# Performance work log

Hardware: AMD Instinct MI355X
Metric: run time of the kernel (lower is better)

The kernel has to match this reference:

```python
import jax, jax.numpy as jnp
import numpy as np

# Hypernetwork config (matches init_kwargs)
INP = 4096      # inp_size
MSK = 64        # mask_size
HID = 64        # node_hidden_size (target-net hidden)
OUT = 10        # out_size (target outputs)
L1, L2, L3 = 64, 256, 128  # hypernet trunk layers
B = 16384       # batch
WVEC = MSK * HID + HID + HID * OUT + OUT  # 4810 generated weights per sample


def _linear_params(key, fan_in, fan_out):
    # torch.nn.Linear default init: U(-1/sqrt(fan_in), 1/sqrt(fan_in))
    lim = 1.0 / np.sqrt(fan_in)
    kw, kb = jax.random.split(key)
    W = jax.random.uniform(kw, (fan_out, fan_in), minval=-lim, maxval=lim, dtype=jnp.float32)
    b = jax.random.uniform(kb, (fan_out,), minval=-lim, maxval=lim, dtype=jnp.float32)
    return W, b


def setup_inputs() -> dict:
    key = jax.random.key(0)
    ks = jax.random.split(key, 6)
    W1, b1 = _linear_params(ks[0], INP, L1)
    W2, b2 = _linear_params(ks[1], L1, L2)
    W3, b3 = _linear_params(ks[2], L2, L3)
    W4, b4 = _linear_params(ks[3], L3, WVEC)
    data = jax.random.normal(ks[4], (B, INP), dtype=jnp.float32)
    mask_idx = jnp.sort(jax.random.randint(ks[5], (B, MSK), 0, INP), axis=1)  # int indices of active features
    return dict(data=data, mask_idx=mask_idx,
                W1=W1, b1=b1, W2=W2, b2=b2, W3=W3, b3=b3, W4=W4, b4=b4)


def reference(data, mask_idx, W1, b1, W2, b2, W3, b3, W4, b4):
    b = data.shape[0]
    # Rebuild the float binary mask [B, INP] from indices (scatter ones)
    rows = jnp.arange(b)[:, None]
    mask = jnp.zeros((b, INP), dtype=data.dtype).at[rows, mask_idx].set(1.0)

    # craft_network: 4-layer MLP on the mask (dropout is identity in eval / for reference)
    h = jax.nn.relu(mask @ W1.T + b1)
    h = jax.nn.relu(h @ W2.T + b2)
    h = jax.nn.relu(h @ W3.T + b3)
    w = h @ W4.T + b4  # [B, WVEC] generated weights per sample

    # Split per-sample generated weights (same layout as InsertableNet)
    iw_end = MSK * HID
    ib_end = iw_end + HID
    ow_end = ib_end + HID * OUT
    inp_w = w[:, :iw_end].reshape(b, HID, MSK)       # [B, H, M]
    inp_b = w[:, iw_end:ib_end]                      # [B, H]
    out_w = w[:, ib_end:ow_end].reshape(b, OUT, HID) # [B, O, H]
    out_b = w[:, ow_end:]                            # [B, O]

    # Per-sample gather of masked features: data[i, mask[i]] -> [B, M]
    xm = jnp.take_along_axis(data, mask_idx, axis=1)

    # Batched tiny 2-layer MLP (replaces the per-sample Python loop)
    hid = jax.nn.relu(jnp.einsum('bhm,bm->bh', inp_w, xm) + inp_b)
    res = jnp.einsum('boh,bh->bo', out_w, hid) + out_b  # [B, OUT]
    return res
```

## Files before the change

### kernel.cpp

```cpp
#include <hip/hip_runtime.h>


typedef _Float16 f16;
typedef _Float16 f16x8 __attribute__((ext_vector_type(8)));
typedef _Float16 f16x4 __attribute__((ext_vector_type(4)));
typedef float    f32x4 __attribute__((ext_vector_type(4)));

#define NPAD 4864

__global__ __launch_bounds__(256) void k_prep(
    const float* __restrict__ W1, const float* __restrict__ W2,
    const float* __restrict__ W3, const float* __restrict__ W4,
    f16* __restrict__ W1Th, f16* __restrict__ W2h,
    f16* __restrict__ W3h, f16* __restrict__ W4s)
{
    const int tid = blockIdx.x * 256 + threadIdx.x;
    const int stride = gridDim.x * 256;
    for (int e = tid; e < 4096 * 64; e += stride) {
        int j = e >> 6, i = e & 63;
        W1Th[e] = (f16)W1[(size_t)i * 4096 + j];
    }
    for (int e = tid; e < NPAD * 128; e += stride) {
        const int j    = e & 7;
        const int lane = (e >> 3) & 63;
        const int mt   = (e >> 9) & 3;
        const int kk   = (e >> 11) & 3;
        const int c    = e >> 13;
        const int lr = lane & 15, g = lane >> 4;
        const int row = 64 * c + 16 * mt + lr;
        const int col = 32 * kk + 8 * g + j;
        W4s[e] = (row < 4810) ? (f16)W4[(size_t)row * 128 + col] : (f16)0.f;
    }
    for (int e = tid; e < 256 * 64; e += stride)  W2h[e] = (f16)W2[e];
    for (int e = tid; e < 128 * 256; e += stride) W3h[e] = (f16)W3[e];
}

__global__ __launch_bounds__(512, 2) void k_main(
    const float* __restrict__ data, const int* __restrict__ midx,
    const f16* __restrict__ W1Th, const float* __restrict__ b1,
    const f16* __restrict__ W2h, const float* __restrict__ b2,
    const f16* __restrict__ W3h, const float* __restrict__ b3,
    const f16* __restrict__ W4s, const float* __restrict__ b4,
    float* __restrict__ out)
{
    __shared__ __align__(16) char uMain[40960];
    __shared__ __align__(16) char uB[17408];
    __shared__ __align__(16) char uC[17408];
    __shared__ __align__(16) float res_s[64 * 12];

    const int t = threadIdx.x, w = t >> 6, lane = t & 63;
    const int lr = lane & 15, g = lane >> 4;
    const int row0 = blockIdx.x * 64;
    const f32x4 zero = {0.f, 0.f, 0.f, 0.f};

    int*   idx_s = (int*)uB;
    char*  h2b   = uMain;
    char*  h1b   = uMain + 32768;
    char*  h3b   = uC;
    float* xm_s  = (float*)uB;
    float* hid_s = (float*)uC;

    for (int e = t; e < 4096; e += 512)
        idx_s[e] = midx[(size_t)row0 * 64 + e];
    __syncthreads();

    float xr[8];
    #pragma unroll
    for (int k = 0; k < 8; ++k) {
        const int e = k * 512 + t;
        xr[k] = data[(size_t)(row0 + (e >> 6)) * 4096 + idx_s[e]];
    }

    {
        const f32x4 b1v = *(const f32x4*)&b1[lr * 4];
        for (int p = 0; p < 4; ++p) {
            const int s0 = 8 * w + 2 * p, s1 = s0 + 1;
            f32x4 a0 = zero, a1 = zero;
            #pragma unroll
            for (int tt = 0; tt < 16; ++tt) {
                const int i = g * 16 + tt;
                const int c0 = idx_s[s0 * 64 + i];
                const int q0 = (i > 0) ? idx_s[s0 * 64 + i - 1] : -1;
                const int c1 = idx_s[s1 * 64 + i];
                const int q1 = (i > 0) ? idx_s[s1 * 64 + i - 1] : -1;
                const f16x4 w0 = *(const f16x4*)&W1Th[c0 * 64 + lr * 4];
                const f16x4 w1 = *(const f16x4*)&W1Th[c1 * 64 + lr * 4];
                #pragma unroll
                for (int q = 0; q < 4; ++q) {
                    a0[q] += (c0 != q0) ? (float)w0[q] : 0.f;
                    a1[q] += (c1 != q1) ? (float)w1[q] : 0.f;
                }
            }
            #pragma unroll
            for (int q = 0; q < 4; ++q) {
                a0[q] += __shfl_xor(a0[q], 16);
                a0[q] += __shfl_xor(a0[q], 32);
                a1[q] += __shfl_xor(a1[q], 16);
                a1[q] += __shfl_xor(a1[q], 32);
            }
            if (g == 0) {
                f16x4 h0, h1v;
                #pragma unroll
                for (int q = 0; q < 4; ++q) {
                    h0[q]  = (f16)fmaxf(a0[q] + b1v[q], 0.f);
                    h1v[q] = (f16)fmaxf(a1[q] + b1v[q], 0.f);
                }
                *(f16x4*)(h1b + ((s0 * 128 + lr * 8) ^ ((s0 & 7) << 4))) = h0;
                *(f16x4*)(h1b + ((s1 * 128 + lr * 8) ^ ((s1 & 7) << 4))) = h1v;
            }
        }
    }
    __syncthreads();

    {
        f16x8 a2[2][2], bh[4][2];
        #pragma unroll
        for (int mt = 0; mt < 2; ++mt)
            #pragma unroll
            for (int kk = 0; kk < 2; ++kk)
                a2[mt][kk] = *(const f16x8*)&W2h[(32 * w + 16 * mt + lr) * 64 + 32 * kk + 8 * g];
        #pragma unroll
        for (int rt = 0; rt < 4; ++rt)
            #pragma unroll
            for (int kk = 0; kk < 2; ++kk) {
                const int s = 16 * rt + lr;
                bh[rt][kk] = *(const f16x8*)(h1b + ((s * 128 + (32 * kk + 8 * g) * 2) ^ ((s & 7) << 4)));
            }

        f32x4 acc2[2][4];
        #pragma unroll
        for (int mt = 0; mt < 2; ++mt)
            #pragma unroll
            for (int rt = 0; rt < 4; ++rt) {
                acc2[mt][rt] = __builtin_amdgcn_mfma_f32_16x16x32_f16(a2[mt][0], bh[rt][0], zero, 0, 0, 0);
                acc2[mt][rt] = __builtin_amdgcn_mfma_f32_16x16x32_f16(a2[mt][1], bh[rt][1], acc2[mt][rt], 0, 0, 0);
            }

        #pragma unroll
        for (int mt = 0; mt < 2; ++mt) {
            const f32x4 bv = *(const f32x4*)&b2[32 * w + 16 * mt + 4 * g];
            #pragma unroll
            for (int rt = 0; rt < 4; ++rt) {
                const int s = 16 * rt + lr;
                f16x4 hv;
                #pragma unroll
                for (int q = 0; q < 4; ++q)
                    hv[q] = (f16)fmaxf(acc2[mt][rt][q] + bv[q], 0.f);
                *(f16x4*)(h2b + ((s * 512 + (32 * w + 16 * mt + 4 * g) * 2) ^ ((s & 7) << 4))) = hv;
            }
        }
    }
    __syncthreads();

    {
        f32x4 acc3[4] = {zero, zero, zero, zero};
        #pragma unroll 2
        for (int kk = 0; kk < 8; ++kk) {
            const f16x8 a3 = *(const f16x8*)&W3h[(16 * w + lr) * 256 + 32 * kk + 8 * g];
            #pragma unroll
            for (int rt = 0; rt < 4; ++rt) {
                const int s = 16 * rt + lr;
                const f16x8 bb = *(const f16x8*)(h2b + ((s * 512 + (32 * kk + 8 * g) * 2) ^ ((s & 7) << 4)));
                acc3[rt] = __builtin_amdgcn_mfma_f32_16x16x32_f16(a3, bb, acc3[rt], 0, 0, 0);
            }
        }
        const f32x4 bv3 = *(const f32x4*)&b3[16 * w + 4 * g];
        #pragma unroll
        for (int rt = 0; rt < 4; ++rt) {
            const int s = 16 * rt + lr;
            f16x4 hv;
            #pragma unroll
            for (int q = 0; q < 4; ++q)
                hv[q] = (f16)fmaxf(acc3[rt][q] + bv3[q], 0.f);
            *(f16x4*)(h3b + ((s * 256 + (16 * w + 4 * g) * 2) ^ ((s & 7) << 4))) = hv;
        }
    }
    __syncthreads();

    #pragma unroll
    for (int k = 0; k < 8; ++k) {
        const int e = k * 512 + t;
        xm_s[(e >> 6) * 68 + (e & 63)] = xr[k];
    }
    f16x8 bfrag[4][4];
    #pragma unroll
    for (int u = 0; u < 4; ++u)
        #pragma unroll
        for (int kk = 0; kk < 4; ++kk) {
            const int s = 16 * u + lr;
            bfrag[kk][u] = *(const f16x8*)(h3b + ((s * 256 + (32 * kk + 8 * g) * 2) ^ ((s & 7) << 4)));
        }
    __syncthreads();

    f16x4 xmr[4][4];
    #pragma unroll
    for (int mt = 0; mt < 4; ++mt)
        #pragma unroll
        for (int u = 0; u < 4; ++u) {
            const f32x4 xv = *(const f32x4*)&xm_s[(16 * u + lr) * 68 + 16 * mt + 4 * g];
            f16x4 xh;
            #pragma unroll
            for (int q = 0; q < 4; ++q) xh[q] = (f16)xv[q];
            xmr[mt][u] = xh;
        }

    const char* W4b = (const char*)W4s;
    const int afoff = lane * 16;

#define LDAF(dst, c, kk) { const char* cb_ = W4b + (size_t)(c) * 16384 + (kk) * 4096 + afoff; \
    dst[0] = *(const f16x8*)(cb_);        dst[1] = *(const f16x8*)(cb_ + 1024); \
    dst[2] = *(const f16x8*)(cb_ + 2048); dst[3] = *(const f16x8*)(cb_ + 3072); }

#define MFMA16(af, kk) { \
    _Pragma("unroll") for (int mt = 0; mt < 4; ++mt) \
    _Pragma("unroll") for (int u = 0; u < 4; ++u) \
        acc[mt][u] = __builtin_amdgcn_mfma_f32_16x16x32_f16(af[mt], bfrag[kk][u], acc[mt][u], 0, 0, 0); }

    {
        f16x8 afA[4], afB[4];
        LDAF(afA, w, 0)
        for (int i = 0; i < 8; ++i) {
            const int c = 8 * i + w;
            f32x4 bv[4];
            #pragma unroll
            for (int mt = 0; mt < 4; ++mt)
                bv[mt] = *(const f32x4*)&b4[64 * c + 16 * mt + 4 * g];
            LDAF(afB, c, 1)
            f32x4 acc[4][4];
            #pragma unroll
            for (int mt = 0; mt < 4; ++mt)
                #pragma unroll
                for (int u = 0; u < 4; ++u)
                    acc[mt][u] = __builtin_amdgcn_mfma_f32_16x16x32_f16(afA[mt], bfrag[0][u], zero, 0, 0, 0);
            LDAF(afA, c, 2)
            MFMA16(afB, 1)
            LDAF(afB, c, 3)
            MFMA16(afA, 2)
            if (i < 7) { LDAF(afA, 8 * (i + 1) + w, 0) }
            MFMA16(afB, 3)

            #pragma unroll
            for (int u = 0; u < 4; ++u) {
                float sum = 0.f;
                #pragma unroll
                for (int mt = 0; mt < 4; ++mt)
                    #pragma unroll
                    for (int q = 0; q < 4; ++q)
                        sum += (acc[mt][u][q] + bv[mt][q]) * (float)xmr[mt][u][q];
                sum += __shfl_xor(sum, 16);
                sum += __shfl_xor(sum, 32);
                if (g == 0) hid_s[(16 * u + lr) * 68 + c] = sum;
            }
        }
    }

    f32x4 acc64[4] = {zero, zero, zero, zero};
    if (w < 4) {
        f16x8 af64[4];
        #pragma unroll
        for (int kk = 0; kk < 4; ++kk)
            af64[kk] = *(const f16x8*)(W4b + (size_t)64 * 16384 + kk * 4096 + w * 1024 + afoff);
        #pragma unroll
        for (int kk = 0; kk < 4; ++kk)
            #pragma unroll
            for (int u = 0; u < 4; ++u)
                acc64[u] = __builtin_amdgcn_mfma_f32_16x16x32_f16(af64[kk], bfrag[kk][u], acc64[u], 0, 0, 0);
    }
    __syncthreads();
    if (w < 4) {
        const f32x4 bv64 = *(const f32x4*)&b4[4096 + 16 * w + 4 * g];
        #pragma unroll
        for (int u = 0; u < 4; ++u) {
            float* hp = &hid_s[(16 * u + lr) * 68 + 16 * w + 4 * g];
            f32x4 hv = *(const f32x4*)hp;
            #pragma unroll
            for (int q = 0; q < 4; ++q)
                hv[q] = hv[q] + acc64[u][q] + bv64[q];
            *(f32x4*)hp = hv;
        }
    }
    __syncthreads();
    for (int e = t; e < 4096; e += 512) {
        const int si = e >> 6, h = e & 63;
        hid_s[si * 68 + h] = fmaxf(hid_s[si * 68 + h], 0.f);
    }
    __syncthreads();
    #pragma unroll
    for (int mt = 0; mt < 4; ++mt)
        #pragma unroll
        for (int u = 0; u < 4; ++u) {
            const f32x4 hv = *(const f32x4*)&hid_s[(16 * u + lr) * 68 + 16 * mt + 4 * g];
            f16x4 xh;
            #pragma unroll
            for (int q = 0; q < 4; ++q) xh[q] = (f16)hv[q];
            xmr[mt][u] = xh;
        }

    auto do_out = [&](int c) {
        f32x4 bv[4];
        #pragma unroll
        for (int mt = 0; mt < 4; ++mt)
            bv[mt] = *(const f32x4*)&b4[64 * c + 16 * mt + 4 * g];
        f16x8 afA[4], afB[4];
        LDAF(afA, c, 0)
        LDAF(afB, c, 1)
        f32x4 acc[4][4];
        #pragma unroll
        for (int mt = 0; mt < 4; ++mt)
            #pragma unroll
            for (int u = 0; u < 4; ++u)
                acc[mt][u] = __builtin_amdgcn_mfma_f32_16x16x32_f16(afA[mt], bfrag[0][u], zero, 0, 0, 0);
        LDAF(afA, c, 2)
        MFMA16(afB, 1)
        LDAF(afB, c, 3)
        MFMA16(afA, 2)
        MFMA16(afB, 3)
        #pragma unroll
        for (int u = 0; u < 4; ++u) {
            float sum = 0.f;
            #pragma unroll
            for (int mt = 0; mt < 4; ++mt)
                #pragma unroll
                for (int q = 0; q < 4; ++q)
                    sum += (acc[mt][u][q] + bv[mt][q]) * (float)xmr[mt][u][q];
            sum += __shfl_xor(sum, 16);
            sum += __shfl_xor(sum, 32);
            if (g == 0) res_s[(16 * u + lr) * 12 + (c - 65)] = sum;
        }
    };
    do_out(65 + w);
    if (w >= 6) do_out(67 + w);

    f32x4 acc75[4] = {zero, zero, zero, zero};
    if (w == 4) {
        f16x8 af75[4];
        #pragma unroll
        for (int kk = 0; kk < 4; ++kk)
            af75[kk] = *(const f16x8*)(W4b + (size_t)75 * 16384 + kk * 4096 + afoff);
        #pragma unroll
        for (int kk = 0; kk < 4; ++kk)
            #pragma unroll
            for (int u = 0; u < 4; ++u)
                acc75[u] = __builtin_amdgcn_mfma_f32_16x16x32_f16(af75[kk], bfrag[kk][u], acc75[u], 0, 0, 0);
    }
    __syncthreads();
    if (w == 4) {
        #pragma unroll
        for (int u = 0; u < 4; ++u)
            #pragma unroll
            for (int q = 0; q < 4; ++q) {
                const int o = 4 * g + q;
                if (o < 10)
                    res_s[(16 * u + lr) * 12 + o] += acc75[u][q] + b4[4800 + o];
            }
    }
    __syncthreads();

    for (int e = t; e < 640; e += 512)
        out[(size_t)row0 * 10 + e] = res_s[(e / 10) * 12 + (e % 10)];
#undef LDAF
#undef MFMA16
}

extern "C" void kernel_launch(void* const* d_in, const int* in_sizes, int n_in,
                              void* d_out, int out_size, void* d_ws, size_t ws_size,
                              hipStream_t stream)
{
    const float* data = (const float*)d_in[0];
    const int*   midx = (const int*)d_in[1];
    const float* W1   = (const float*)d_in[2];
    const float* b1   = (const float*)d_in[3];
    const float* W2   = (const float*)d_in[4];
    const float* b2   = (const float*)d_in[5];
    const float* W3   = (const float*)d_in[6];
    const float* b3   = (const float*)d_in[7];
    const float* W4   = (const float*)d_in[8];
    const float* b4   = (const float*)d_in[9];
    float* out = (float*)d_out;

    f16* W1Th = (f16*)d_ws;
    f16* W4s  = W1Th + (size_t)4096 * 64;
    f16* W2h  = W4s + (size_t)NPAD * 128;
    f16* W3h  = W2h + 256 * 64;

    k_prep<<<512, 256, 0, stream>>>(W1, W2, W3, W4, W1Th, W2h, W3h, W4s);
    k_main<<<256, 512, 0, stream>>>(data, midx, W1Th, b1, W2h, b2, W3h, b3,
                                    W4s, b4, out);
}
```

Before: 78.46 us.

## Split fused kernel into front MLP kernel and W4 GEMM kernel

The monolithic kernel is split into two. k_front computes the mask MLP layers 1-3 over 16-row tiles with 1024 blocks, so more blocks run in parallel across the CUs, and writes the gathered features and h3 to workspace. k_gemm then loads those from global memory and performs the generated-weight GEMM and the tiny per-sample MLP. This trades an extra launch and a global round trip for h3 and xm (a few MB) for better occupancy and parallelism in the front stages.

Result: slower. 91.88 us (+17.1%).

```diff
diff --git a/kernel.cpp b/kernel.cpp
--- a/kernel.cpp
+++ b/kernel.cpp
@@ -35,46 +35,38 @@
     for (int e = tid; e < 128 * 256; e += stride) W3h[e] = (f16)W3[e];
 }
 
-__global__ __launch_bounds__(512, 2) void k_main(
+__global__ __launch_bounds__(256, 4) void k_front(
     const float* __restrict__ data, const int* __restrict__ midx,
     const f16* __restrict__ W1Th, const float* __restrict__ b1,
     const f16* __restrict__ W2h, const float* __restrict__ b2,
     const f16* __restrict__ W3h, const float* __restrict__ b3,
-    const f16* __restrict__ W4s, const float* __restrict__ b4,
-    float* __restrict__ out)
+    float* __restrict__ xm_ws, f16* __restrict__ h3h)
 {
-    __shared__ __align__(16) char uMain[40960];
-    __shared__ __align__(16) char uB[17408];
-    __shared__ __align__(16) char uC[17408];
-    __shared__ __align__(16) float res_s[64 * 12];
+    __shared__ __align__(16) int  idx_s[16 * 64];
+    __shared__ __align__(16) char h1b[2048];
+    __shared__ __align__(16) char h2b[8192];
 
     const int t = threadIdx.x, w = t >> 6, lane = t & 63;
     const int lr = lane & 15, g = lane >> 4;
-    const int row0 = blockIdx.x * 64;
+    const int row0 = blockIdx.x * 16;
     const f32x4 zero = {0.f, 0.f, 0.f, 0.f};
 
-    int*   idx_s = (int*)uB;
-    char*  h2b   = uMain;
-    char*  h1b   = uMain + 32768;
-    char*  h3b   = uC;
-    float* xm_s  = (float*)uB;
-    float* hid_s = (float*)uC;
-
-    for (int e = t; e < 4096; e += 512)
-        idx_s[e] = midx[(size_t)row0 * 64 + e];
-    __syncthreads();
-
-    float xr[8];
-    #pragma unroll
-    for (int k = 0; k < 8; ++k) {
-        const int e = k * 512 + t;
+    for (int k = 0; k < 4; ++k)
+        idx_s[k * 256 + t] = midx[(size_t)row0 * 64 + k * 256 + t];
+    __syncthreads();
+
+    float xr[4];
+    #pragma unroll
+    for (int k = 0; k < 4; ++k) {
+        const int e = k * 256 + t;
         xr[k] = data[(size_t)(row0 + (e >> 6)) * 4096 + idx_s[e]];
     }
 
     {
         const f32x4 b1v = *(const f32x4*)&b1[lr * 4];
-        for (int p = 0; p < 4; ++p) {
-            const int s0 = 8 * w + 2 * p, s1 = s0 + 1;
+        #pragma unroll
+        for (int p = 0; p < 2; ++p) {
+            const int s0 = 4 * w + 2 * p, s1 = s0 + 1;
             f32x4 a0 = zero, a1 = zero;
             #pragma unroll
             for (int tt = 0; tt < 16; ++tt) {
@@ -110,94 +102,93 @@
             }
         }
     }
+    #pragma unroll
+    for (int k = 0; k < 4; ++k) {
+        const int e = k * 256 + t;
+        xm_ws[(size_t)(row0 + (e >> 6)) * 64 + (e & 63)] = xr[k];
+    }
     __syncthreads();
 
     {
-        f16x8 a2[2][2], bh[4][2];
-        #pragma unroll
-        for (int mt = 0; mt < 2; ++mt)
+        f16x8 a2[4][2], bh[2];
+        #pragma unroll
+        for (int mt = 0; mt < 4; ++mt)
             #pragma unroll
             for (int kk = 0; kk < 2; ++kk)
-                a2[mt][kk] = *(const f16x8*)&W2h[(32 * w + 16 * mt + lr) * 64 + 32 * kk + 8 * g];
-        #pragma unroll
-        for (int rt = 0; rt < 4; ++rt)
-            #pragma unroll
-            for (int kk = 0; kk < 2; ++kk) {
-                const int s = 16 * rt + lr;
-                bh[rt][kk] = *(const f16x8*)(h1b + ((s * 128 + (32 * kk + 8 * g) * 2) ^ ((s & 7) << 4)));
-            }
-
-        f32x4 acc2[2][4];
-        #pragma unroll
-        for (int mt = 0; mt < 2; ++mt)
-            #pragma unroll
-            for (int rt = 0; rt < 4; ++rt) {
-                acc2[mt][rt] = __builtin_amdgcn_mfma_f32_16x16x32_f16(a2[mt][0], bh[rt][0], zero, 0, 0, 0);
-                acc2[mt][rt] = __builtin_amdgcn_mfma_f32_16x16x32_f16(a2[mt][1], bh[rt][1], acc2[mt][rt], 0, 0, 0);
-            }
-
-        #pragma unroll
-        for (int mt = 0; mt < 2; ++mt) {
-            const f32x4 bv = *(const f32x4*)&b2[32 * w + 16 * mt + 4 * g];
-            #pragma unroll
-            for (int rt = 0; rt < 4; ++rt) {
-                const int s = 16 * rt + lr;
-                f16x4 hv;
-                #pragma unroll
-                for (int q = 0; q < 4; ++q)
-                    hv[q] = (f16)fmaxf(acc2[mt][rt][q] + bv[q], 0.f);
-                *(f16x4*)(h2b + ((s * 512 + (32 * w + 16 * mt + 4 * g) * 2) ^ ((s & 7) << 4))) = hv;
-            }
+                a2[mt][kk] = *(const f16x8*)&W2h[(64 * w + 16 * mt + lr) * 64 + 32 * kk + 8 * g];
+        #pragma unroll
+        for (int kk = 0; kk < 2; ++kk)
+            bh[kk] = *(const f16x8*)(h1b + ((lr * 128 + (32 * kk + 8 * g) * 2) ^ ((lr & 7) << 4)));
+
+        f32x4 acc2[4];
+        #pragma unroll
+        for (int mt = 0; mt < 4; ++mt) {
+            acc2[mt] = __builtin_amdgcn_mfma_f32_16x16x32_f16(a2[mt][0], bh[0], zero, 0, 0, 0);
+            acc2[mt] = __builtin_amdgcn_mfma_f32_16x16x32_f16(a2[mt][1], bh[1], acc2[mt], 0, 0, 0);
+        }
+        #pragma unroll
+        for (int mt = 0; mt < 4; ++mt) {
+            const int n = 64 * w + 16 * mt + 4 * g;
+            const f32x4 bv = *(const f32x4*)&b2[n];
+            f16x4 hv;
+            #pragma unroll
+            for (int q = 0; q < 4; ++q)
+                hv[q] = (f16)fmaxf(acc2[mt][q] + bv[q], 0.f);
+            *(f16x4*)(h2b + ((lr * 512 + n * 2) ^ ((lr & 7) << 4))) = hv;
         }
     }
     __syncthreads();
 
     {
-        f32x4 acc3[4] = {zero, zero, zero, zero};
+        f32x4 acc3[2] = {zero, zero};
         #pragma unroll 2
         for (int kk = 0; kk < 8; ++kk) {
-            const f16x8 a3 = *(const f16x8*)&W3h[(16 * w + lr) * 256 + 32 * kk + 8 * g];
-            #pragma unroll
-            for (int rt = 0; rt < 4; ++rt) {
-                const int s = 16 * rt + lr;
-                const f16x8 bb = *(const f16x8*)(h2b + ((s * 512 + (32 * kk + 8 * g) * 2) ^ ((s & 7) << 4)));
-                acc3[rt] = __builtin_amdgcn_mfma_f32_16x16x32_f16(a3, bb, acc3[rt], 0, 0, 0);
-            }
-        }
-        const f32x4 bv3 = *(const f32x4*)&b3[16 * w + 4 * g];
-        #pragma unroll
-        for (int rt = 0; rt < 4; ++rt) {
-            const int s = 16 * rt + lr;
+            const f16x8 bb = *(const f16x8*)(h2b + ((lr * 512 + (32 * kk + 8 * g) * 2) ^ ((lr & 7) << 4)));
+            #pragma unroll
+            for (int mt = 0; mt < 2; ++mt) {
+                const f16x8 a3 = *(const f16x8*)&W3h[(32 * w + 16 * mt + lr) * 256 + 32 * kk + 8 * g];
+                acc3[mt] = __builtin_amdgcn_mfma_f32_16x16x32_f16(a3, bb, acc3[mt], 0, 0, 0);
+            }
+        }
+        #pragma unroll
+        for (int mt = 0; mt < 2; ++mt) {
+            const int n = 32 * w + 16 * mt + 4 * g;
+            const f32x4 bv3 = *(const f32x4*)&b3[n];
             f16x4 hv;
             #pragma unroll
             for (int q = 0; q < 4; ++q)
-                hv[q] = (f16)fmaxf(acc3[rt][q] + bv3[q], 0.f);
-            *(f16x4*)(h3b + ((s * 256 + (16 * w + 4 * g) * 2) ^ ((s & 7) << 4))) = hv;
-        }
-    }
-    __syncthreads();
-
-    #pragma unroll
-    for (int k = 0; k < 8; ++k) {
-        const int e = k * 512 + t;
-        xm_s[(e >> 6) * 68 + (e & 63)] = xr[k];
-    }
+                hv[q] = (f16)fmaxf(acc3[mt][q] + bv3[q], 0.f);
+            *(f16x4*)&h3h[(size_t)(row0 + lr) * 128 + n] = hv;
+        }
+    }
+}
+
+__global__ __launch_bounds__(512, 2) void k_gemm(
+    const float* __restrict__ xm_ws, const f16* __restrict__ h3h,
+    const f16* __restrict__ W4s, const float* __restrict__ b4,
+    float* __restrict__ out)
+{
+    __shared__ __align__(16) float hid_s[64 * 68];
+    __shared__ __align__(16) float res_s[64 * 12];
+
+    const int t = threadIdx.x, w = t >> 6, lane = t & 63;
+    const int lr = lane & 15, g = lane >> 4;
+    const int row0 = blockIdx.x * 64;
+    const f32x4 zero = {0.f, 0.f, 0.f, 0.f};
+
     f16x8 bfrag[4][4];
     #pragma unroll
     for (int u = 0; u < 4; ++u)
         #pragma unroll
-        for (int kk = 0; kk < 4; ++kk) {
-            const int s = 16 * u + lr;
-            bfrag[kk][u] = *(const f16x8*)(h3b + ((s * 256 + (32 * kk + 8 * g) * 2) ^ ((s & 7) << 4)));
-        }
-    __syncthreads();
+        for (int kk = 0; kk < 4; ++kk)
+            bfrag[kk][u] = *(const f16x8*)&h3h[(size_t)(row0 + 16 * u + lr) * 128 + 32 * kk + 8 * g];
 
     f16x4 xmr[4][4];
     #pragma unroll
     for (int mt = 0; mt < 4; ++mt)
         #pragma unroll
         for (int u = 0; u < 4; ++u) {
-            const f32x4 xv = *(const f32x4*)&xm_s[(16 * u + lr) * 68 + 16 * mt + 4 * g];
+            const f32x4 xv = *(const f32x4*)&xm_ws[(size_t)(row0 + 16 * u + lr) * 64 + 16 * mt + 4 * g];
             f16x4 xh;
             #pragma unroll
             for (int q = 0; q < 4; ++q) xh[q] = (f16)xv[q];
@@ -378,12 +369,15 @@
     const float* b4   = (const float*)d_in[9];
     float* out = (float*)d_out;
 
-    f16* W1Th = (f16*)d_ws;
-    f16* W4s  = W1Th + (size_t)4096 * 64;
-    f16* W2h  = W4s + (size_t)NPAD * 128;
-    f16* W3h  = W2h + 256 * 64;
-
-    k_prep<<<512, 256, 0, stream>>>(W1, W2, W3, W4, W1Th, W2h, W3h, W4s);
-    k_main<<<256, 512, 0, stream>>>(data, midx, W1Th, b1, W2h, b2, W3h, b3,
-                                    W4s, b4, out);
+    float* xm_ws = (float*)d_ws;
+    f16*   W1Th  = (f16*)(xm_ws + (size_t)16384 * 64);
+    f16*   W4s   = W1Th + (size_t)4096 * 64;
+    f16*   W2h   = W4s + (size_t)NPAD * 128;
+    f16*   W3h   = W2h + 256 * 64;
+    f16*   h3h   = W3h + 128 * 256;
+
+    k_prep <<<512, 256, 0, stream>>>(W1, W2, W3, W4, W1Th, W2h, W3h, W4s);
+    k_front<<<1024, 256, 0, stream>>>(data, midx, W1Th, b1, W2h, b2, W3h, b3,
+                                      xm_ws, h3h);
+    k_gemm <<<256, 512, 0, stream>>>(xm_ws, h3h, W4s, b4, out);
 }
```

## Dedicate one wave to data gather while seven waves run trunk MLP

Applied to the files above, without the earlier changes.

Wave 7 now performs the whole per-row masked-feature gather from global memory (64 loads per lane) while waves 0-6 compute the first three trunk layers, redistributing layer work across 7 waves. The 64-row hidden-weight chunk is now computed inside the main loop and staged in shared memory, and the bias-row contribution goes to a separate buffer. This removes several __syncthreads (replaced with lighter LDS-only barriers) and aims to hide gather latency behind compute. In exchange it drops the register-aliased shared buffers, so shared memory use grows and may reduce occupancy from the 2-blocks target. Wave 7 also holds 64 floats of gather results in registers, and the trunk work is unevenly split across the seven compute waves.

New measurement: 74.89 us, median of 2. 4.6% less time.

```diff
diff --git a/kernel.cpp b/kernel.cpp
--- a/kernel.cpp
+++ b/kernel.cpp
@@ -7,6 +7,10 @@
 typedef float    f32x4 __attribute__((ext_vector_type(4)));
 
 #define NPAD 4864
+
+#define BAR() do { asm volatile("s_waitcnt lgkmcnt(0)" ::: "memory"); \
+                   __builtin_amdgcn_s_barrier();                      \
+                   asm volatile("" ::: "memory"); } while (0)
 
 __global__ __launch_bounds__(256) void k_prep(
     const float* __restrict__ W1, const float* __restrict__ W2,
@@ -43,38 +47,36 @@
     const f16* __restrict__ W4s, const float* __restrict__ b4,
     float* __restrict__ out)
 {
-    __shared__ __align__(16) char uMain[40960];
-    __shared__ __align__(16) char uB[17408];
-    __shared__ __align__(16) char uC[17408];
+    __shared__ __align__(16) int   idx_s[64 * 64];
+    __shared__ __align__(16) char  h1b[8192];
+    __shared__ __align__(16) char  h2b[32768];
+    __shared__ __align__(16) char  h3b[16384];
+    __shared__ __align__(16) float xm_s[64 * 68];
+    __shared__ __align__(16) float hid_s[64 * 68];
+    __shared__ __align__(16) f16   w64_s[64 * 64];
     __shared__ __align__(16) float res_s[64 * 12];
+    __shared__ __align__(16) float res_b[64 * 12];
 
     const int t = threadIdx.x, w = t >> 6, lane = t & 63;
     const int lr = lane & 15, g = lane >> 4;
     const int row0 = blockIdx.x * 64;
     const f32x4 zero = {0.f, 0.f, 0.f, 0.f};
 
-    int*   idx_s = (int*)uB;
-    char*  h2b   = uMain;
-    char*  h1b   = uMain + 32768;
-    char*  h3b   = uC;
-    float* xm_s  = (float*)uB;
-    float* hid_s = (float*)uC;
-
     for (int e = t; e < 4096; e += 512)
         idx_s[e] = midx[(size_t)row0 * 64 + e];
-    __syncthreads();
-
-    float xr[8];
-    #pragma unroll
-    for (int k = 0; k < 8; ++k) {
-        const int e = k * 512 + t;
-        xr[k] = data[(size_t)(row0 + (e >> 6)) * 4096 + idx_s[e]];
-    }
-
-    {
+    BAR();
+
+    float xr[64];
+
+    if (w == 7) {
+        #pragma unroll
+        for (int k = 0; k < 64; ++k)
+            xr[k] = data[(size_t)(row0 + k) * 4096 + idx_s[k * 64 + lane]];
+        __builtin_amdgcn_sched_barrier(0);
+    } else {
         const f32x4 b1v = *(const f32x4*)&b1[lr * 4];
-        for (int p = 0; p < 4; ++p) {
-            const int s0 = 8 * w + 2 * p, s1 = s0 + 1;
+        for (int sp = w; sp < 32; sp += 7) {
+            const int s0 = 2 * sp, s1 = s0 + 1;
             f32x4 a0 = zero, a1 = zero;
             #pragma unroll
             for (int tt = 0; tt < 16; ++tt) {
@@ -110,15 +112,10 @@
             }
         }
     }
-    __syncthreads();
-
-    {
-        f16x8 a2[2][2], bh[4][2];
-        #pragma unroll
-        for (int mt = 0; mt < 2; ++mt)
-            #pragma unroll
-            for (int kk = 0; kk < 2; ++kk)
-                a2[mt][kk] = *(const f16x8*)&W2h[(32 * w + 16 * mt + lr) * 64 + 32 * kk + 8 * g];
+    BAR();
+
+    if (w < 7) {
+        f16x8 bh[4][2];
         #pragma unroll
         for (int rt = 0; rt < 4; ++rt)
             #pragma unroll
@@ -126,62 +123,67 @@
                 const int s = 16 * rt + lr;
                 bh[rt][kk] = *(const f16x8*)(h1b + ((s * 128 + (32 * kk + 8 * g) * 2) ^ ((s & 7) << 4)));
             }
-
-        f32x4 acc2[2][4];
-        #pragma unroll
-        for (int mt = 0; mt < 2; ++mt)
-            #pragma unroll
-            for (int rt = 0; rt < 4; ++rt) {
-                acc2[mt][rt] = __builtin_amdgcn_mfma_f32_16x16x32_f16(a2[mt][0], bh[rt][0], zero, 0, 0, 0);
-                acc2[mt][rt] = __builtin_amdgcn_mfma_f32_16x16x32_f16(a2[mt][1], bh[rt][1], acc2[mt][rt], 0, 0, 0);
-            }
-
-        #pragma unroll
-        for (int mt = 0; mt < 2; ++mt) {
-            const f32x4 bv = *(const f32x4*)&b2[32 * w + 16 * mt + 4 * g];
+        for (int nb = w; nb < 8; nb += 7) {
+            const int n0 = 32 * nb;
+            f16x8 a2[2][2];
+            #pragma unroll
+            for (int mt = 0; mt < 2; ++mt)
+                #pragma unroll
+                for (int kk = 0; kk < 2; ++kk)
+                    a2[mt][kk] = *(const f16x8*)&W2h[(n0 + 16 * mt + lr) * 64 + 32 * kk + 8 * g];
+            f32x4 acc2[2][4];
+            #pragma unroll
+            for (int mt = 0; mt < 2; ++mt)
+                #pragma unroll
+                for (int rt = 0; rt < 4; ++rt) {
+                    acc2[mt][rt] = __builtin_amdgcn_mfma_f32_16x16x32_f16(a2[mt][0], bh[rt][0], zero, 0, 0, 0);
+                    acc2[mt][rt] = __builtin_amdgcn_mfma_f32_16x16x32_f16(a2[mt][1], bh[rt][1], acc2[mt][rt], 0, 0, 0);
+                }
+            #pragma unroll
+            for (int mt = 0; mt < 2; ++mt) {
+                const f32x4 bv = *(const f32x4*)&b2[n0 + 16 * mt + 4 * g];
+                #pragma unroll
+                for (int rt = 0; rt < 4; ++rt) {
+                    const int s = 16 * rt + lr;
+                    f16x4 hv;
+                    #pragma unroll
+                    for (int q = 0; q < 4; ++q)
+                        hv[q] = (f16)fmaxf(acc2[mt][rt][q] + bv[q], 0.f);
+                    *(f16x4*)(h2b + ((s * 512 + (n0 + 16 * mt + 4 * g) * 2) ^ ((s & 7) << 4))) = hv;
+                }
+            }
+        }
+    }
+    BAR();
+
+    if (w < 7) {
+        for (int nb = w; nb < 8; nb += 7) {
+            const int n0 = 16 * nb;
+            f32x4 acc3[4] = {zero, zero, zero, zero};
+            #pragma unroll 2
+            for (int kk = 0; kk < 8; ++kk) {
+                const f16x8 a3 = *(const f16x8*)&W3h[(n0 + lr) * 256 + 32 * kk + 8 * g];
+                #pragma unroll
+                for (int rt = 0; rt < 4; ++rt) {
+                    const int s = 16 * rt + lr;
+                    const f16x8 bb = *(const f16x8*)(h2b + ((s * 512 + (32 * kk + 8 * g) * 2) ^ ((s & 7) << 4)));
+                    acc3[rt] = __builtin_amdgcn_mfma_f32_16x16x32_f16(a3, bb, acc3[rt], 0, 0, 0);
+                }
+            }
+            const f32x4 bv3 = *(const f32x4*)&b3[n0 + 4 * g];
             #pragma unroll
             for (int rt = 0; rt < 4; ++rt) {
                 const int s = 16 * rt + lr;
                 f16x4 hv;
                 #pragma unroll
                 for (int q = 0; q < 4; ++q)
-                    hv[q] = (f16)fmaxf(acc2[mt][rt][q] + bv[q], 0.f);
-                *(f16x4*)(h2b + ((s * 512 + (32 * w + 16 * mt + 4 * g) * 2) ^ ((s & 7) << 4))) = hv;
-            }
-        }
-    }
-    __syncthreads();
-
-    {
-        f32x4 acc3[4] = {zero, zero, zero, zero};
-        #pragma unroll 2
-        for (int kk = 0; kk < 8; ++kk) {
-            const f16x8 a3 = *(const f16x8*)&W3h[(16 * w + lr) * 256 + 32 * kk + 8 * g];
-            #pragma unroll
-            for (int rt = 0; rt < 4; ++rt) {
-                const int s = 16 * rt + lr;
-                const f16x8 bb = *(const f16x8*)(h2b + ((s * 512 + (32 * kk + 8 * g) * 2) ^ ((s & 7) << 4)));
-                acc3[rt] = __builtin_amdgcn_mfma_f32_16x16x32_f16(a3, bb, acc3[rt], 0, 0, 0);
-            }
-        }
-        const f32x4 bv3 = *(const f32x4*)&b3[16 * w + 4 * g];
-        #pragma unroll
-        for (int rt = 0; rt < 4; ++rt) {
-            const int s = 16 * rt + lr;
-            f16x4 hv;
-            #pragma unroll
-            for (int q = 0; q < 4; ++q)
-                hv[q] = (f16)fmaxf(acc3[rt][q] + bv3[q], 0.f);
-            *(f16x4*)(h3b + ((s * 256 + (16 * w + 4 * g) * 2) ^ ((s & 7) << 4))) = hv;
-        }
-    }
-    __syncthreads();
-
-    #pragma unroll
-    for (int k = 0; k < 8; ++k) {
-        const int e = k * 512 + t;
-        xm_s[(e >> 6) * 68 + (e & 63)] = xr[k];
-    }
+                    hv[q] = (f16)fmaxf(acc3[rt][q] + bv3[q], 0.f);
+                *(f16x4*)(h3b + ((s * 256 + (n0 + 4 * g) * 2) ^ ((s & 7) << 4))) = hv;
+            }
+        }
+    }
+    BAR();
+
     f16x8 bfrag[4][4];
     #pragma unroll
     for (int u = 0; u < 4; ++u)
@@ -190,7 +192,12 @@
             const int s = 16 * u + lr;
             bfrag[kk][u] = *(const f16x8*)(h3b + ((s * 256 + (32 * kk + 8 * g) * 2) ^ ((s & 7) << 4)));
         }
-    __syncthreads();
+    if (w == 7) {
+        #pragma unroll
+        for (int k = 0; k < 64; ++k)
+            xm_s[k * 68 + lane] = xr[k];
+    }
+    BAR();
 
     f16x4 xmr[4][4];
     #pragma unroll
@@ -216,29 +223,28 @@
     _Pragma("unroll") for (int u = 0; u < 4; ++u) \
         acc[mt][u] = __builtin_amdgcn_mfma_f32_16x16x32_f16(af[mt], bfrag[kk][u], acc[mt][u], 0, 0, 0); }
 
-    {
+    for (int c = w; c < 65; c += 8) {
         f16x8 afA[4], afB[4];
-        LDAF(afA, w, 0)
-        for (int i = 0; i < 8; ++i) {
-            const int c = 8 * i + w;
-            f32x4 bv[4];
-            #pragma unroll
-            for (int mt = 0; mt < 4; ++mt)
-                bv[mt] = *(const f32x4*)&b4[64 * c + 16 * mt + 4 * g];
-            LDAF(afB, c, 1)
-            f32x4 acc[4][4];
-            #pragma unroll
-            for (int mt = 0; mt < 4; ++mt)
-                #pragma unroll
-                for (int u = 0; u < 4; ++u)
-                    acc[mt][u] = __builtin_amdgcn_mfma_f32_16x16x32_f16(afA[mt], bfrag[0][u], zero, 0, 0, 0);
-            LDAF(afA, c, 2)
-            MFMA16(afB, 1)
-            LDAF(afB, c, 3)
-            MFMA16(afA, 2)
-            if (i < 7) { LDAF(afA, 8 * (i + 1) + w, 0) }
-            MFMA16(afB, 3)
-
+        LDAF(afA, c, 0)
+        LDAF(afB, c, 1)
+        f32x4 acc[4][4];
+        #pragma unroll
+        for (int mt = 0; mt < 4; ++mt)
+            #pragma unroll
+            for (int u = 0; u < 4; ++u)
+                acc[mt][u] = __builtin_amdgcn_mfma_f32_16x16x32_f16(afA[mt], bfrag[0][u], zero, 0, 0, 0);
+        LDAF(afA, c, 2)
+        MFMA16(afB, 1)
+        LDAF(afB, c, 3)
+        MFMA16(afA, 2)
+        MFMA16(afB, 3)
+
+        f32x4 bv[4];
+        #pragma unroll
+        for (int mt = 0; mt < 4; ++mt)
+            bv[mt] = *(const f32x4*)&b4[64 * c + 16 * mt + 4 * g];
+
+        if (c < 64) {
             #pragma unroll
             for (int u = 0; u < 4; ++u) {
                 float sum = 0.f;
@@ -251,49 +257,34 @@
                 sum += __shfl_xor(sum, 32);
                 if (g == 0) hid_s[(16 * u + lr) * 68 + c] = sum;
             }
-        }
-    }
-
-    f32x4 acc64[4] = {zero, zero, zero, zero};
-    if (w < 4) {
-        f16x8 af64[4];
-        #pragma unroll
-        for (int kk = 0; kk < 4; ++kk)
-            af64[kk] = *(const f16x8*)(W4b + (size_t)64 * 16384 + kk * 4096 + w * 1024 + afoff);
-        #pragma unroll
-        for (int kk = 0; kk < 4; ++kk)
+        } else {
             #pragma unroll
             for (int u = 0; u < 4; ++u)
-                acc64[u] = __builtin_amdgcn_mfma_f32_16x16x32_f16(af64[kk], bfrag[kk][u], acc64[u], 0, 0, 0);
-    }
-    __syncthreads();
-    if (w < 4) {
-        const f32x4 bv64 = *(const f32x4*)&b4[4096 + 16 * w + 4 * g];
-        #pragma unroll
-        for (int u = 0; u < 4; ++u) {
-            float* hp = &hid_s[(16 * u + lr) * 68 + 16 * w + 4 * g];
-            f32x4 hv = *(const f32x4*)hp;
-            #pragma unroll
-            for (int q = 0; q < 4; ++q)
-                hv[q] = hv[q] + acc64[u][q] + bv64[q];
-            *(f32x4*)hp = hv;
-        }
-    }
-    __syncthreads();
-    for (int e = t; e < 4096; e += 512) {
-        const int si = e >> 6, h = e & 63;
-        hid_s[si * 68 + h] = fmaxf(hid_s[si * 68 + h], 0.f);
-    }
-    __syncthreads();
+                #pragma unroll
+                for (int mt = 0; mt < 4; ++mt) {
+                    f16x4 wv;
+                    #pragma unroll
+                    for (int q = 0; q < 4; ++q)
+                        wv[q] = (f16)(acc[mt][u][q] + bv[mt][q]);
+                    *(f16x4*)&w64_s[(16 * u + lr) * 64 + 16 * mt + 4 * g] = wv;
+                }
+        }
+    }
+    BAR();
+
+    f16x4 hidr[4][4];
     #pragma unroll
     for (int mt = 0; mt < 4; ++mt)
         #pragma unroll
         for (int u = 0; u < 4; ++u) {
-            const f32x4 hv = *(const f32x4*)&hid_s[(16 * u + lr) * 68 + 16 * mt + 4 * g];
+            const int s = 16 * u + lr;
             f16x4 xh;
             #pragma unroll
-            for (int q = 0; q < 4; ++q) xh[q] = (f16)hv[q];
-            xmr[mt][u] = xh;
+            for (int q = 0; q < 4; ++q) {
+                const int h = 16 * mt + 4 * g + q;
+                xh[q] = (f16)fmaxf(hid_s[s * 68 + h] + (float)w64_s[s * 64 + h], 0.f);
+            }
+            hidr[mt][u] = xh;
         }
 
     auto do_out = [&](int c) {
@@ -322,42 +313,38 @@
             for (int mt = 0; mt < 4; ++mt)
                 #pragma unroll
                 for (int q = 0; q < 4; ++q)
-                    sum += (acc[mt][u][q] + bv[mt][q]) * (float)xmr[mt][u][q];
+                    sum += (acc[mt][u][q] + bv[mt][q]) * (float)hidr[mt][u][q];
             sum += __shfl_xor(sum, 16);
             sum += __shfl_xor(sum, 32);
             if (g == 0) res_s[(16 * u + lr) * 12 + (c - 65)] = sum;
         }
     };
     do_out(65 + w);
-    if (w >= 6) do_out(67 + w);
-
-    f32x4 acc75[4] = {zero, zero, zero, zero};
-    if (w == 4) {
-        f16x8 af75[4];
-        #pragma unroll
-        for (int kk = 0; kk < 4; ++kk)
-            af75[kk] = *(const f16x8*)(W4b + (size_t)75 * 16384 + kk * 4096 + afoff);
-        #pragma unroll
-        for (int kk = 0; kk < 4; ++kk)
+    if (w < 2) do_out(73 + w);
+
+    if (w == 2) {
+        f32x4 accb[4] = {zero, zero, zero, zero};
+        #pragma unroll
+        for (int kk = 0; kk < 4; ++kk) {
+            const f16x8 af = *(const f16x8*)(W4b + (size_t)75 * 16384 + kk * 4096 + afoff);
             #pragma unroll
             for (int u = 0; u < 4; ++u)
-                acc75[u] = __builtin_amdgcn_mfma_f32_16x16x32_f16(af75[kk], bfrag[kk][u], acc75[u], 0, 0, 0);
-    }
-    __syncthreads();
-    if (w == 4) {
+                accb[u] = __builtin_amdgcn_mfma_f32_16x16x32_f16(af, bfrag[kk][u], accb[u], 0, 0, 0);
+        }
         #pragma unroll
         for (int u = 0; u < 4; ++u)
             #pragma unroll
             for (int q = 0; q < 4; ++q) {
                 const int o = 4 * g + q;
                 if (o < 10)
-                    res_s[(16 * u + lr) * 12 + o] += acc75[u][q] + b4[4800 + o];
-            }
-    }
-    __syncthreads();
+                    res_b[(16 * u + lr) * 12 + o] = accb[u][q] + b4[4800 + o];
+            }
+    }
+    BAR();
 
     for (int e = t; e < 640; e += 512)
-        out[(size_t)row0 * 10 + e] = res_s[(e / 10) * 12 + (e % 10)];
+        out[(size_t)row0 * 10 + e] =
+            res_s[(e / 10) * 12 + (e % 10)] + res_b[(e / 10) * 12 + (e % 10)];
 #undef LDAF
 #undef MFMA16
 }
```
